# Kernel optimization log

Measured on AMD Instinct MI355X. Metric: run time of the kernel, lower is better.

## Reference

```python
import jax, jax.numpy as jnp
import numpy as np

N_HEAD = 8

def _l2norm(x, eps=1e-12):
    # F.normalize(p=2, dim=-1): x / max(||x||_2, eps)
    return x / jnp.maximum(jnp.linalg.norm(x, axis=-1, keepdims=True), eps)

def setup_inputs() -> dict:
    key = jax.random.key(0)
    ks = jax.random.split(key, 9)
    B, L, E = 2, 2048, 512
    s = 0.02
    return {
        "query": jax.random.normal(ks[0], (B, L, E), dtype=jnp.float32),
        "Wq": s * jax.random.normal(ks[1], (E, E), dtype=jnp.float32),
        "bq": jnp.zeros((E,), dtype=jnp.float32),
        "Wk": s * jax.random.normal(ks[2], (E, E), dtype=jnp.float32),
        "bk": jnp.zeros((E,), dtype=jnp.float32),
        "Wv": s * jax.random.normal(ks[3], (E, E), dtype=jnp.float32),
        "bv": jnp.zeros((E,), dtype=jnp.float32),
        "Wo": s * jax.random.normal(ks[4], (E, E), dtype=jnp.float32),
        "bo": jnp.zeros((E,), dtype=jnp.float32),
    }

def reference(query, Wq, bq, Wk, bk, Wv, bv, Wo, bo):
    B, L, E = query.shape
    H = N_HEAD
    hd = E // H
    # Faithful to torch: .view(tgt_len, bsz, E) is a RESHAPE, not a transpose.
    x = query.reshape(L, B, E)
    q = jax.nn.relu(x @ Wq.T + bq)
    k = jax.nn.relu(x @ Wk.T + bk)
    v = x @ Wv.T + bv
    q = _l2norm(q)
    k = _l2norm(k)
    # (L, B, E) -> (L, B*H, hd) -> (B*H, L, hd)
    q_ = q.reshape(L, B * H, hd).transpose(1, 0, 2)
    k_ = k.reshape(L, B * H, hd).transpose(1, 0, 2)
    v_ = v.reshape(L, B * H, hd).transpose(1, 0, 2)
    # Causal linear attention: cumulative outer-product of k,v then contract with q.
    kv = jnp.einsum('nld,nlm->nldm', k_, v_)      # [B*H, L, hd, hd]
    kv_cum = jnp.cumsum(kv, axis=1)
    out = jnp.einsum('nld,nldm->nlm', q_, kv_cum)  # [B*H, L, hd]
    out = out.transpose(1, 0, 2).reshape(L, B, E)
    out = out @ Wo.T + bo
    return out.reshape(B, L, E)
```

## Files before the change

kernel.cpp:

```cpp
#include <hip/hip_runtime.h>
#include <hip/hip_bf16.h>

typedef __attribute__((ext_vector_type(8))) short short8;
typedef __attribute__((ext_vector_type(4))) float f32x4;
using bf16 = __hip_bfloat16;

__device__ __forceinline__ unsigned short f2bf(float f) {
    unsigned u = __float_as_uint(f);
    u += 0x7fff + ((u >> 16) & 1);
    return (unsigned short)(u >> 16);
}
__device__ __forceinline__ float bf2f(unsigned short s) {
    return __uint_as_float(((unsigned)s) << 16);
}
__device__ __forceinline__ void gl_lds16(const unsigned short* g, unsigned short* l) {
    __builtin_amdgcn_global_load_lds(
        (const __attribute__((address_space(1))) unsigned int*)g,
        (__attribute__((address_space(3))) unsigned int*)l, 16, 0, 0);
}


__global__ __launch_bounds__(256) void pack_kernel(
    const float* __restrict__ X, const float* __restrict__ Wq, const float* __restrict__ Wk,
    const float* __restrict__ Wv, const float* __restrict__ Wo,
    bf16* __restrict__ Xp, bf16* __restrict__ Wqp, bf16* __restrict__ Wkp,
    bf16* __restrict__ Wvp, bf16* __restrict__ Wop, float* __restrict__ ssq)
{
    __shared__ __align__(16) unsigned short sm[4096];
    int id = blockIdx.x;
    int tid = threadIdx.x;
    if (id < 8) {
        int zi = id * 1024 + tid * 4;
        *(float4*)&ssq[zi] = make_float4(0.f, 0.f, 0.f, 0.f);
    }
    const float* src; unsigned short* dst; int g, sc;
    if (id < 512) { src = X; dst = (unsigned short*)Xp; g = id >> 3; sc = id & 7; }
    else {
        int t = id - 512; int wsel = t >> 6; int u = t & 63;
        g = u >> 3; sc = u & 7;
        src = (wsel == 0) ? Wq : ((wsel == 1) ? Wk : ((wsel == 2) ? Wv : Wo));
        dst = (unsigned short*)((wsel == 0) ? Wqp : ((wsel == 1) ? Wkp : ((wsel == 2) ? Wvp : Wop)));
    }
    int r = tid >> 2, kq = tid & 3;
    const float* sp = src + (size_t)(g * 64 + r) * 512 + sc * 64 + kq * 16;
    #pragma unroll
    for (int i = 0; i < 4; ++i) {
        float4 v = *(const float4*)(sp + i * 4);
        int kk = kq * 16 + i * 4;
        int sl = kk >> 3, el = kk & 7;
        ushort4 u4;
        u4.x = f2bf(v.x); u4.y = f2bf(v.y); u4.z = f2bf(v.z); u4.w = f2bf(v.w);
        *(ushort4*)&sm[(sl * 64 + r) * 8 + el] = u4;
    }
    __syncthreads();
    unsigned short* dp = dst + (size_t)g * 32768 + sc * 4096;
    *(uint4*)(dp + tid * 16)     = *(const uint4*)&sm[tid * 16];
    *(uint4*)(dp + tid * 16 + 8) = *(const uint4*)&sm[tid * 16 + 8];
}

__global__ __launch_bounds__(256) void qkv_gemm_kernel(
    const bf16* __restrict__ Xp,
    const bf16* __restrict__ W0p, const bf16* __restrict__ W1p, const bf16* __restrict__ W2p,
    const float* __restrict__ b0, const float* __restrict__ b1, const float* __restrict__ b2,
    bf16* __restrict__ O0, bf16* __restrict__ O1, bf16* __restrict__ O2,
    float* __restrict__ ssq)
{
    __shared__ __align__(16) unsigned short smem[8192];
    unsigned short* As = smem;
    unsigned short* Bs = smem + 2048;
    int z = blockIdx.z;
    const unsigned short* Wg = (const unsigned short*)((z == 0) ? W0p : ((z == 1) ? W1p : W2p));
    const float* bias = (z == 0) ? b0 : ((z == 1) ? b1 : b2);
    unsigned short* Out = (unsigned short*)((z == 0) ? O0 : ((z == 1) ? O1 : O2));
    const unsigned short* Ag = (const unsigned short*)Xp;

    int g  = blockIdx.x;
    int gB = blockIdx.y * 2;
    int m0 = g * 64;
    int n0 = blockIdx.y * 128;
    int tid = threadIdx.x;
    int lane = tid & 63;
    int w = tid >> 6;
    int wm = (w >> 1) * 32;
    int wn = (w & 1) * 64;
    int fr = lane & 15, qf = lane >> 4;

    f32x4 zero4 = {0.f, 0.f, 0.f, 0.f};
    f32x4 acc[2][4];
    #pragma unroll
    for (int t = 0; t < 2; ++t)
        #pragma unroll
        for (int u = 0; u < 4; ++u) acc[t][u] = zero4;

    for (int kw = 0; kw < 16; ++kw) {
        int s0 = kw * 4;
        __syncthreads();
        gl_lds16(Ag + ((size_t)(g * 64 + s0 + w) * 64 + lane) * 8, As + w * 512);
        gl_lds16(Wg + ((size_t)(gB * 64 + s0 + w) * 64 + lane) * 8, Bs + w * 1024);
        gl_lds16(Wg + ((size_t)((gB + 1) * 64 + s0 + w) * 64 + lane) * 8, Bs + w * 1024 + 512);
        __syncthreads();
        short8 af[2], bfr[4];
        #pragma unroll
        for (int t = 0; t < 2; ++t) af[t] = *(const short8*)&As[(qf * 64 + wm + t * 16 + fr) * 8];
        #pragma unroll
        for (int u = 0; u < 4; ++u) bfr[u] = *(const short8*)&Bs[(qf * 128 + wn + u * 16 + fr) * 8];
        #pragma unroll
        for (int t = 0; t < 2; ++t)
            #pragma unroll
            for (int u = 0; u < 4; ++u)
                acc[t][u] = __builtin_amdgcn_mfma_f32_16x16x32_bf16(af[t], bfr[u], acc[t][u], 0, 0, 0);
    }

    bool relu = (z < 2);
    int rb = qf * 4;
    #pragma unroll
    for (int t = 0; t < 2; ++t)
        #pragma unroll
        for (int u = 0; u < 4; ++u) {
            float bv = bias[n0 + wn + u * 16 + fr];
            #pragma unroll
            for (int r = 0; r < 4; ++r) {
                float v = acc[t][u][r] + bv;
                if (relu) v = fmaxf(v, 0.f);
                acc[t][u][r] = v;
            }
        }
    if (relu) {
        #pragma unroll
        for (int t = 0; t < 2; ++t)
            #pragma unroll
            for (int r = 0; r < 4; ++r) {
                float s = 0.f;
                #pragma unroll
                for (int u = 0; u < 4; ++u) s += acc[t][u][r] * acc[t][u][r];
                #pragma unroll
                for (int off = 1; off < 16; off <<= 1) s += __shfl_xor(s, off, 64);
                if (fr == 0) atomicAdd(&ssq[z * 4096 + m0 + wm + t * 16 + rb + r], s);
            }
    }
    __syncthreads();
    #pragma unroll
    for (int t = 0; t < 2; ++t)
        #pragma unroll
        for (int u = 0; u < 4; ++u)
            #pragma unroll
            for (int r = 0; r < 4; ++r)
                smem[(wm + t * 16 + rb + r) * 128 + wn + u * 16 + fr] = f2bf(acc[t][u][r]);
    __syncthreads();
    #pragma unroll
    for (int rep = 0; rep < 4; ++rep) {
        int idx8 = rep * 256 + tid;
        int row = idx8 >> 4, col8 = (idx8 & 15) * 8;
        *(uint4*)(Out + (size_t)(m0 + row) * 512 + n0 + col8) = *(const uint4*)&smem[row * 128 + col8];
    }
}

__global__ __launch_bounds__(256) void chunk_kv_kernel(
    const bf16* __restrict__ Kb, const bf16* __restrict__ Vb,
    const float* __restrict__ ssq, float* __restrict__ ScT, bf16* __restrict__ Vt_g)
{
    int n = blockIdx.x >> 4, c = blockIdx.x & 15;
    int b = n >> 3, h = n & 7;
    __shared__ float Ks[64 * 64];
    __shared__ float Vs[64 * 64];
    const unsigned short* Kg = (const unsigned short*)Kb;
    const unsigned short* Vg = (const unsigned short*)Vb;
    int tid = threadIdx.x;
    int td = tid >> 4, tm = tid & 15;
    int d0 = td * 4, m0 = tm * 4;
    int vm = tid & 63, vj0 = (tid >> 6) * 16;
    float acc[4][4] = {};
    for (int half = 0; half < 2; ++half) {
        __syncthreads();
        #pragma unroll
        for (int rep = 0; rep < 4; ++rep) {
            int idx = rep * 1024 + tid * 4;
            int j = idx >> 6, d = idx & 63;
            int grow = (c * 128 + half * 64 + j) * 2 + b;
            ushort4 ku = *(const ushort4*)&Kg[(size_t)grow * 512 + h * 64 + d];
            ushort4 vu = *(const ushort4*)&Vg[(size_t)grow * 512 + h * 64 + d];
            float rk = 1.f / fmaxf(sqrtf(ssq[4096 + grow]), 1e-12f);
            *(float4*)&Ks[j * 64 + d] = make_float4(bf2f(ku.x), bf2f(ku.y), bf2f(ku.z), bf2f(ku.w));
            *(float4*)&Vs[j * 64 + d] = make_float4(bf2f(vu.x) * rk, bf2f(vu.y) * rk,
                                                    bf2f(vu.z) * rk, bf2f(vu.w) * rk);
        }
        __syncthreads();
        for (int j = 0; j < 64; ++j) {
            float4 kv = *(const float4*)&Ks[j * 64 + d0];
            float4 vv = *(const float4*)&Vs[j * 64 + m0];
            acc[0][0] += kv.x*vv.x; acc[0][1] += kv.x*vv.y; acc[0][2] += kv.x*vv.z; acc[0][3] += kv.x*vv.w;
            acc[1][0] += kv.y*vv.x; acc[1][1] += kv.y*vv.y; acc[1][2] += kv.y*vv.z; acc[1][3] += kv.y*vv.w;
            acc[2][0] += kv.z*vv.x; acc[2][1] += kv.z*vv.y; acc[2][2] += kv.z*vv.z; acc[2][3] += kv.z*vv.w;
            acc[3][0] += kv.w*vv.x; acc[3][1] += kv.w*vv.y; acc[3][2] += kv.w*vv.z; acc[3][3] += kv.w*vv.w;
        }
        unsigned short tmp[16];
        #pragma unroll
        for (int i = 0; i < 16; ++i) tmp[i] = f2bf(Vs[(vj0 + i) * 64 + vm]);
        size_t vtoff = (size_t)n * 131072 + (size_t)vm * 2048 + c * 128 + half * 64 + vj0;
        *(uint4*)((unsigned short*)Vt_g + vtoff)     = *(uint4*)&tmp[0];
        *(uint4*)((unsigned short*)Vt_g + vtoff + 8) = *(uint4*)&tmp[8];
    }
    float* outp = ScT + (size_t)blockIdx.x * 4096;
    #pragma unroll
    for (int j2 = 0; j2 < 4; ++j2) {
        float4 o4 = make_float4(acc[0][j2], acc[1][j2], acc[2][j2], acc[3][j2]);
        *(float4*)&outp[(m0 + j2) * 64 + d0] = o4;
    }
}

__global__ __launch_bounds__(256) void prefix_kernel(const float* __restrict__ ScT, bf16* __restrict__ SpT)
{
    int n = blockIdx.x >> 4;
    int idx = ((blockIdx.x & 15) << 8) + threadIdx.x;
    size_t base = (size_t)n * 65536 + idx;
    unsigned short* sp = (unsigned short*)SpT;
    float run = 0.f;
    #pragma unroll
    for (int c = 0; c < 16; ++c) {
        size_t off = base + (size_t)c * 4096;
        sp[off] = f2bf(run);
        run += ScT[off];
    }
}

__global__ __launch_bounds__(256) void attn_kernel(
    const bf16* __restrict__ Qb, const bf16* __restrict__ Kb,
    const bf16* __restrict__ Vt_g, const bf16* __restrict__ SpT_g,
    const float* __restrict__ ssq, bf16* __restrict__ AOb)
{
    int n = blockIdx.x >> 4, c = blockIdx.x & 15;
    int b = n >> 3, h = n & 7;
    __shared__ unsigned short Qs[128 * 72];
    __shared__ unsigned short Ks[128 * 72];
    __shared__ unsigned short Vt[64 * 136];
    __shared__ unsigned short Ps[4 * 32 * 40];
    int tid = threadIdx.x;
    int lane = tid & 63;
    int w = tid >> 6;
    int fr = lane & 15, q = lane >> 4;

    const unsigned short* Qg = (const unsigned short*)Qb;
    const unsigned short* Kg = (const unsigned short*)Kb;
    const unsigned short* Vg = (const unsigned short*)Vt_g;

    #pragma unroll
    for (int rep = 0; rep < 4; ++rep) {
        int idx = rep * 256 + tid;
        int l = idx >> 3, dc = (idx & 7) * 8;
        size_t goff = (size_t)((c * 128 + l) * 2 + b) * 512 + h * 64 + dc;
        *(uint4*)&Qs[l * 72 + dc] = *(const uint4*)(Qg + goff);
        *(uint4*)&Ks[l * 72 + dc] = *(const uint4*)(Kg + goff);
    }
    #pragma unroll
    for (int rep = 0; rep < 4; ++rep) {
        int idx = rep * 256 + tid;
        int m = idx >> 4, jc = (idx & 15) * 8;
        *(uint4*)&Vt[m * 136 + jc] =
            *(const uint4*)(Vg + (size_t)n * 131072 + (size_t)m * 2048 + c * 128 + jc);
    }
    __syncthreads();

    short8 qf[2][2];
    #pragma unroll
    for (int lt = 0; lt < 2; ++lt)
        #pragma unroll
        for (int kh = 0; kh < 2; ++kh)
            qf[lt][kh] = *(const short8*)&Qs[(w * 32 + lt * 16 + fr) * 72 + kh * 32 + q * 8];

    f32x4 zero4 = {0.f, 0.f, 0.f, 0.f};
    f32x4 oacc[2][4];
    #pragma unroll
    for (int lt = 0; lt < 2; ++lt)
        #pragma unroll
        for (int mt = 0; mt < 4; ++mt) oacc[lt][mt] = zero4;

    const unsigned short* spg = (const unsigned short*)SpT_g + (size_t)blockIdx.x * 4096;
    #pragma unroll
    for (int mt = 0; mt < 4; ++mt) {
        #pragma unroll
        for (int kh = 0; kh < 2; ++kh) {
            short8 sf = *(const short8*)&spg[(mt * 16 + fr) * 64 + kh * 32 + q * 8];
            oacc[0][mt] = __builtin_amdgcn_mfma_f32_16x16x32_bf16(qf[0][kh], sf, oacc[0][mt], 0, 0, 0);
            oacc[1][mt] = __builtin_amdgcn_mfma_f32_16x16x32_bf16(qf[1][kh], sf, oacc[1][mt], 0, 0, 0);
        }
    }

    unsigned short* myPs = &Ps[w * 1280];
    int rbase = q * 4;
    for (int jt = 0; jt <= w; ++jt) {
        f32x4 pacc[2][2];
        pacc[0][0] = zero4; pacc[0][1] = zero4; pacc[1][0] = zero4; pacc[1][1] = zero4;
        #pragma unroll
        for (int jt16 = 0; jt16 < 2; ++jt16) {
            #pragma unroll
            for (int kh = 0; kh < 2; ++kh) {
                short8 kf = *(const short8*)&Ks[(jt * 32 + jt16 * 16 + fr) * 72 + kh * 32 + q * 8];
                pacc[0][jt16] = __builtin_amdgcn_mfma_f32_16x16x32_bf16(qf[0][kh], kf, pacc[0][jt16], 0, 0, 0);
                pacc[1][jt16] = __builtin_amdgcn_mfma_f32_16x16x32_bf16(qf[1][kh], kf, pacc[1][jt16], 0, 0, 0);
            }
        }
        bool diag = (jt == w);
        #pragma unroll
        for (int lt = 0; lt < 2; ++lt)
            #pragma unroll
            for (int jt16 = 0; jt16 < 2; ++jt16)
                #pragma unroll
                for (int r = 0; r < 4; ++r) {
                    int ll = lt * 16 + rbase + r;
                    int jl = jt16 * 16 + fr;
                    float pv = pacc[lt][jt16][r];
                    if (diag && jl > ll) pv = 0.f;
                    myPs[ll * 40 + jl] = f2bf(pv);
                }
        short8 pf0 = *(const short8*)&myPs[fr * 40 + q * 8];
        short8 pf1 = *(const short8*)&myPs[(16 + fr) * 40 + q * 8];
        #pragma unroll
        for (int mt = 0; mt < 4; ++mt) {
            short8 vf = *(const short8*)&Vt[(mt * 16 + fr) * 136 + jt * 32 + q * 8];
            oacc[0][mt] = __builtin_amdgcn_mfma_f32_16x16x32_bf16(pf0, vf, oacc[0][mt], 0, 0, 0);
            oacc[1][mt] = __builtin_amdgcn_mfma_f32_16x16x32_bf16(pf1, vf, oacc[1][mt], 0, 0, 0);
        }
    }

    float rqv[2][4];
    #pragma unroll
    for (int lt = 0; lt < 2; ++lt)
        #pragma unroll
        for (int r = 0; r < 4; ++r) {
            int flat = (c * 128 + w * 32 + lt * 16 + rbase + r) * 2 + b;
            rqv[lt][r] = 1.f / fmaxf(sqrtf(ssq[flat]), 1e-12f);
        }
    __syncthreads();
    #pragma unroll
    for (int lt = 0; lt < 2; ++lt)
        #pragma unroll
        for (int mt = 0; mt < 4; ++mt)
            #pragma unroll
            for (int r = 0; r < 4; ++r)
                Qs[(w * 32 + lt * 16 + rbase + r) * 64 + mt * 16 + fr] = f2bf(oacc[lt][mt][r] * rqv[lt][r]);
    __syncthreads();
    #pragma unroll
    for (int rep = 0; rep < 4; ++rep) {
        int idx8 = rep * 256 + tid;
        int l = idx8 >> 3, m8 = (idx8 & 7) * 8;
        *(uint4*)((unsigned short*)AOb + (size_t)((c * 128 + l) * 2 + b) * 512 + h * 64 + m8) =
            *(const uint4*)&Qs[l * 64 + m8];
    }
}

__global__ __launch_bounds__(256) void oproj_kernel(
    const bf16* __restrict__ A, const bf16* __restrict__ Wop,
    const float* __restrict__ bias, float* __restrict__ Out)
{
    __shared__ __align__(16) unsigned short smem[16384];
    unsigned short* As = smem;
    unsigned short* Bs = smem + 2560;
    const unsigned short* Ag = (const unsigned short*)A;
    const unsigned short* Wg = (const unsigned short*)Wop;
    int m0 = blockIdx.x * 64;
    int gB = blockIdx.y * 2;
    int n0 = blockIdx.y * 128;
    int tid = threadIdx.x;
    int lane = tid & 63;
    int w = tid >> 6;
    int fr = lane & 15, qf = lane >> 4;
    int wm = (w >> 1) * 32;
    int wn = (w & 1) * 64;
    int srow = tid >> 2;
    int skk  = (tid & 3) * 8;

    f32x4 zero4 = {0.f, 0.f, 0.f, 0.f};
    f32x4 acc[2][4];
    #pragma unroll
    for (int t = 0; t < 2; ++t)
        #pragma unroll
        for (int u = 0; u < 4; ++u) acc[t][u] = zero4;

    for (int kw = 0; kw < 16; ++kw) {
        int k0 = kw * 32, s0 = kw * 4;
        __syncthreads();
        *(uint4*)&As[srow * 40 + skk] = *(const uint4*)(Ag + (size_t)(m0 + srow) * 512 + k0 + skk);
        gl_lds16(Wg + ((size_t)(gB * 64 + s0 + w) * 64 + lane) * 8, Bs + w * 1024);
        gl_lds16(Wg + ((size_t)((gB + 1) * 64 + s0 + w) * 64 + lane) * 8, Bs + w * 1024 + 512);
        __syncthreads();
        short8 af[2], bfr[4];
        #pragma unroll
        for (int t = 0; t < 2; ++t) af[t] = *(const short8*)&As[(wm + t * 16 + fr) * 40 + qf * 8];
        #pragma unroll
        for (int u = 0; u < 4; ++u) bfr[u] = *(const short8*)&Bs[(qf * 128 + wn + u * 16 + fr) * 8];
        #pragma unroll
        for (int t = 0; t < 2; ++t)
            #pragma unroll
            for (int u = 0; u < 4; ++u)
                acc[t][u] = __builtin_amdgcn_mfma_f32_16x16x32_bf16(af[t], bfr[u], acc[t][u], 0, 0, 0);
    }

    int rb = qf * 4;
    float* Cf = (float*)smem;
    __syncthreads();
    #pragma unroll
    for (int t = 0; t < 2; ++t)
        #pragma unroll
        for (int u = 0; u < 4; ++u) {
            float bv = bias[n0 + wn + u * 16 + fr];
            #pragma unroll
            for (int r = 0; r < 4; ++r)
                Cf[(wm + t * 16 + rb + r) * 128 + wn + u * 16 + fr] = acc[t][u][r] + bv;
        }
    __syncthreads();
    #pragma unroll
    for (int rep = 0; rep < 8; ++rep) {
        int idx = rep * 256 + tid;
        int row = idx >> 5, c4 = (idx & 31) * 4;
        *(float4*)(Out + (size_t)(m0 + row) * 512 + n0 + c4) = *(const float4*)&Cf[row * 128 + c4];
    }
}

extern "C" void kernel_launch(void* const* d_in, const int* in_sizes, int n_in,
                              void* d_out, int out_size, void* d_ws, size_t ws_size,
                              hipStream_t stream)
{
    (void)in_sizes; (void)n_in; (void)out_size; (void)ws_size;
    const float* x  = (const float*)d_in[0];
    const float* Wq = (const float*)d_in[1];
    const float* bq = (const float*)d_in[2];
    const float* Wk = (const float*)d_in[3];
    const float* bk = (const float*)d_in[4];
    const float* Wv = (const float*)d_in[5];
    const float* bv = (const float*)d_in[6];
    const float* Wo = (const float*)d_in[7];
    const float* bo = (const float*)d_in[8];
    float* out = (float*)d_out;

    float* ssq = (float*)d_ws;
    bf16* Xp  = (bf16*)(ssq + 8192);
    bf16* Wqp = Xp + 2097152;
    bf16* Wkp = Wqp + 262144;
    bf16* Wvp = Wkp + 262144;
    bf16* Wop = Wvp + 262144;
    bf16* Qb  = Wop + 262144;
    bf16* Kb  = Qb + 2097152;
    bf16* Vb  = Kb + 2097152;
    bf16* Vt  = Vb + 2097152;
    bf16* AOb = Vt + 2097152;
    bf16* SpT = AOb + 2097152;
    float* ScT = (float*)(SpT + 1048576);

    pack_kernel<<<768, 256, 0, stream>>>(x, Wq, Wk, Wv, Wo, Xp, Wqp, Wkp, Wvp, Wop, ssq);
    qkv_gemm_kernel<<<dim3(64, 4, 3), 256, 0, stream>>>(Xp, Wqp, Wkp, Wvp, bq, bk, bv, Qb, Kb, Vb, ssq);
    chunk_kv_kernel<<<dim3(256), 256, 0, stream>>>(Kb, Vb, ssq, ScT, Vt);
    prefix_kernel<<<dim3(256), 256, 0, stream>>>(ScT, SpT);
    attn_kernel<<<dim3(256), 256, 0, stream>>>(Qb, Kb, Vt, SpT, ssq, AOb);
    oproj_kernel<<<dim3(64, 4), 256, 0, stream>>>(AOb, Wop, bo, out);
}
```

Baseline: 123.6 us.

## Fuse QKV projections per block and fold prefix scan into attention kernel

The QKV GEMM now computes all three projections in one block, sharing each loaded X tile across Wq, Wk and Wv. That cuts A-tile reloads and the grid from 768 to 256 blocks, at the cost of three times the accumulator registers. The separate prefix-sum kernel is removed; each attention block instead sums the preceding chunk states directly from fp32 ScT. This saves a launch and an intermediate bf16 buffer but adds redundant loads that grow with the chunk index.

```diff
diff --git a/kernel.cpp b/kernel.cpp
--- a/kernel.cpp
+++ b/kernel.cpp
@@ -65,14 +65,11 @@
     bf16* __restrict__ O0, bf16* __restrict__ O1, bf16* __restrict__ O2,
     float* __restrict__ ssq)
 {
-    __shared__ __align__(16) unsigned short smem[8192];
-    unsigned short* As = smem;
-    unsigned short* Bs = smem + 2048;
-    int z = blockIdx.z;
-    const unsigned short* Wg = (const unsigned short*)((z == 0) ? W0p : ((z == 1) ? W1p : W2p));
-    const float* bias = (z == 0) ? b0 : ((z == 1) ? b1 : b2);
-    unsigned short* Out = (unsigned short*)((z == 0) ? O0 : ((z == 1) ? O1 : O2));
+    __shared__ __align__(16) unsigned short SM[14336];
+    unsigned short* As = SM;
     const unsigned short* Ag = (const unsigned short*)Xp;
+    const unsigned short* Wg[3] = { (const unsigned short*)W0p, (const unsigned short*)W1p,
+                                    (const unsigned short*)W2p };
 
     int g  = blockIdx.x;
     int gB = blockIdx.y * 2;
@@ -83,75 +80,90 @@
     int w = tid >> 6;
     int wm = (w >> 1) * 32;
     int wn = (w & 1) * 64;
-    int fr = lane & 15, qf = lane >> 4;
+    int fr = lane & 15, q = lane >> 4;
 
     f32x4 zero4 = {0.f, 0.f, 0.f, 0.f};
-    f32x4 acc[2][4];
-    #pragma unroll
-    for (int t = 0; t < 2; ++t)
-        #pragma unroll
-        for (int u = 0; u < 4; ++u) acc[t][u] = zero4;
+    f32x4 acc[3][2][4];
+    #pragma unroll
+    for (int z = 0; z < 3; ++z)
+        #pragma unroll
+        for (int t = 0; t < 2; ++t)
+            #pragma unroll
+            for (int u = 0; u < 4; ++u) acc[z][t][u] = zero4;
 
     for (int kw = 0; kw < 16; ++kw) {
         int s0 = kw * 4;
         __syncthreads();
         gl_lds16(Ag + ((size_t)(g * 64 + s0 + w) * 64 + lane) * 8, As + w * 512);
-        gl_lds16(Wg + ((size_t)(gB * 64 + s0 + w) * 64 + lane) * 8, Bs + w * 1024);
-        gl_lds16(Wg + ((size_t)((gB + 1) * 64 + s0 + w) * 64 + lane) * 8, Bs + w * 1024 + 512);
-        __syncthreads();
-        short8 af[2], bfr[4];
-        #pragma unroll
-        for (int t = 0; t < 2; ++t) af[t] = *(const short8*)&As[(qf * 64 + wm + t * 16 + fr) * 8];
-        #pragma unroll
-        for (int u = 0; u < 4; ++u) bfr[u] = *(const short8*)&Bs[(qf * 128 + wn + u * 16 + fr) * 8];
+        #pragma unroll
+        for (int z = 0; z < 3; ++z) {
+            unsigned short* Bz = SM + 2048 + z * 4096;
+            gl_lds16(Wg[z] + ((size_t)(gB * 64 + s0 + w) * 64 + lane) * 8, Bz + w * 1024);
+            gl_lds16(Wg[z] + ((size_t)((gB + 1) * 64 + s0 + w) * 64 + lane) * 8, Bz + w * 1024 + 512);
+        }
+        __syncthreads();
+        short8 af[2];
+        #pragma unroll
+        for (int t = 0; t < 2; ++t) af[t] = *(const short8*)&As[(q * 64 + wm + t * 16 + fr) * 8];
+        #pragma unroll
+        for (int z = 0; z < 3; ++z) {
+            unsigned short* Bz = SM + 2048 + z * 4096;
+            short8 bfr[4];
+            #pragma unroll
+            for (int u = 0; u < 4; ++u) bfr[u] = *(const short8*)&Bz[(q * 128 + wn + u * 16 + fr) * 8];
+            #pragma unroll
+            for (int t = 0; t < 2; ++t)
+                #pragma unroll
+                for (int u = 0; u < 4; ++u)
+                    acc[z][t][u] = __builtin_amdgcn_mfma_f32_16x16x32_bf16(af[t], bfr[u], acc[z][t][u], 0, 0, 0);
+        }
+    }
+
+    int rb = q * 4;
+    for (int z = 0; z < 3; ++z) {
+        const float* bias = (z == 0) ? b0 : ((z == 1) ? b1 : b2);
+        unsigned short* Out = (unsigned short*)((z == 0) ? O0 : ((z == 1) ? O1 : O2));
+        bool relu = (z < 2);
         #pragma unroll
         for (int t = 0; t < 2; ++t)
             #pragma unroll
+            for (int u = 0; u < 4; ++u) {
+                float bv = bias[n0 + wn + u * 16 + fr];
+                #pragma unroll
+                for (int r = 0; r < 4; ++r) {
+                    float v = acc[z][t][u][r] + bv;
+                    if (relu) v = fmaxf(v, 0.f);
+                    acc[z][t][u][r] = v;
+                }
+            }
+        if (relu) {
+            #pragma unroll
+            for (int t = 0; t < 2; ++t)
+                #pragma unroll
+                for (int r = 0; r < 4; ++r) {
+                    float s = 0.f;
+                    #pragma unroll
+                    for (int u = 0; u < 4; ++u) s += acc[z][t][u][r] * acc[z][t][u][r];
+                    #pragma unroll
+                    for (int off = 1; off < 16; off <<= 1) s += __shfl_xor(s, off, 64);
+                    if (fr == 0) atomicAdd(&ssq[z * 4096 + m0 + wm + t * 16 + rb + r], s);
+                }
+        }
+        __syncthreads();
+        #pragma unroll
+        for (int t = 0; t < 2; ++t)
+            #pragma unroll
             for (int u = 0; u < 4; ++u)
-                acc[t][u] = __builtin_amdgcn_mfma_f32_16x16x32_bf16(af[t], bfr[u], acc[t][u], 0, 0, 0);
-    }
-
-    bool relu = (z < 2);
-    int rb = qf * 4;
-    #pragma unroll
-    for (int t = 0; t < 2; ++t)
-        #pragma unroll
-        for (int u = 0; u < 4; ++u) {
-            float bv = bias[n0 + wn + u * 16 + fr];
-            #pragma unroll
-            for (int r = 0; r < 4; ++r) {
-                float v = acc[t][u][r] + bv;
-                if (relu) v = fmaxf(v, 0.f);
-                acc[t][u][r] = v;
-            }
-        }
-    if (relu) {
-        #pragma unroll
-        for (int t = 0; t < 2; ++t)
-            #pragma unroll
-            for (int r = 0; r < 4; ++r) {
-                float s = 0.f;
                 #pragma unroll
-                for (int u = 0; u < 4; ++u) s += acc[t][u][r] * acc[t][u][r];
-                #pragma unroll
-                for (int off = 1; off < 16; off <<= 1) s += __shfl_xor(s, off, 64);
-                if (fr == 0) atomicAdd(&ssq[z * 4096 + m0 + wm + t * 16 + rb + r], s);
-            }
-    }
-    __syncthreads();
-    #pragma unroll
-    for (int t = 0; t < 2; ++t)
-        #pragma unroll
-        for (int u = 0; u < 4; ++u)
-            #pragma unroll
-            for (int r = 0; r < 4; ++r)
-                smem[(wm + t * 16 + rb + r) * 128 + wn + u * 16 + fr] = f2bf(acc[t][u][r]);
-    __syncthreads();
-    #pragma unroll
-    for (int rep = 0; rep < 4; ++rep) {
-        int idx8 = rep * 256 + tid;
-        int row = idx8 >> 4, col8 = (idx8 & 15) * 8;
-        *(uint4*)(Out + (size_t)(m0 + row) * 512 + n0 + col8) = *(const uint4*)&smem[row * 128 + col8];
+                for (int r = 0; r < 4; ++r)
+                    SM[(wm + t * 16 + rb + r) * 128 + wn + u * 16 + fr] = f2bf(acc[z][t][u][r]);
+        __syncthreads();
+        #pragma unroll
+        for (int rep = 0; rep < 4; ++rep) {
+            int idx8 = rep * 256 + tid;
+            int row = idx8 >> 4, col8 = (idx8 & 15) * 8;
+            *(uint4*)(Out + (size_t)(m0 + row) * 512 + n0 + col8) = *(const uint4*)&SM[row * 128 + col8];
+        }
     }
 }
 
@@ -208,24 +220,9 @@
     }
 }
 
-__global__ __launch_bounds__(256) void prefix_kernel(const float* __restrict__ ScT, bf16* __restrict__ SpT)
-{
-    int n = blockIdx.x >> 4;
-    int idx = ((blockIdx.x & 15) << 8) + threadIdx.x;
-    size_t base = (size_t)n * 65536 + idx;
-    unsigned short* sp = (unsigned short*)SpT;
-    float run = 0.f;
-    #pragma unroll
-    for (int c = 0; c < 16; ++c) {
-        size_t off = base + (size_t)c * 4096;
-        sp[off] = f2bf(run);
-        run += ScT[off];
-    }
-}
-
 __global__ __launch_bounds__(256) void attn_kernel(
     const bf16* __restrict__ Qb, const bf16* __restrict__ Kb,
-    const bf16* __restrict__ Vt_g, const bf16* __restrict__ SpT_g,
+    const bf16* __restrict__ Vt_g, const float* __restrict__ ScT,
     const float* __restrict__ ssq, bf16* __restrict__ AOb)
 {
     int n = blockIdx.x >> 4, c = blockIdx.x & 15;
@@ -274,12 +271,23 @@
         #pragma unroll
         for (int mt = 0; mt < 4; ++mt) oacc[lt][mt] = zero4;
 
-    const unsigned short* spg = (const unsigned short*)SpT_g + (size_t)blockIdx.x * 4096;
+    const float* scb = ScT + (size_t)(n * 16) * 4096;
     #pragma unroll
     for (int mt = 0; mt < 4; ++mt) {
         #pragma unroll
         for (int kh = 0; kh < 2; ++kh) {
-            short8 sf = *(const short8*)&spg[(mt * 16 + fr) * 64 + kh * 32 + q * 8];
+            float sp[8] = {0.f,0.f,0.f,0.f,0.f,0.f,0.f,0.f};
+            int eo = (mt * 16 + fr) * 64 + kh * 32 + q * 8;
+            for (int cp = 0; cp < c; ++cp) {
+                float4 a = *(const float4*)&scb[cp * 4096 + eo];
+                float4 d = *(const float4*)&scb[cp * 4096 + eo + 4];
+                sp[0]+=a.x; sp[1]+=a.y; sp[2]+=a.z; sp[3]+=a.w;
+                sp[4]+=d.x; sp[5]+=d.y; sp[6]+=d.z; sp[7]+=d.w;
+            }
+            unsigned short su[8];
+            #pragma unroll
+            for (int e = 0; e < 8; ++e) su[e] = f2bf(sp[e]);
+            short8 sf = *(const short8*)su;
             oacc[0][mt] = __builtin_amdgcn_mfma_f32_16x16x32_bf16(qf[0][kh], sf, oacc[0][mt], 0, 0, 0);
             oacc[1][mt] = __builtin_amdgcn_mfma_f32_16x16x32_bf16(qf[1][kh], sf, oacc[1][mt], 0, 0, 0);
         }
@@ -443,13 +451,11 @@
     bf16* Vb  = Kb + 2097152;
     bf16* Vt  = Vb + 2097152;
     bf16* AOb = Vt + 2097152;
-    bf16* SpT = AOb + 2097152;
-    float* ScT = (float*)(SpT + 1048576);
+    float* ScT = (float*)(AOb + 2097152);
 
     pack_kernel<<<768, 256, 0, stream>>>(x, Wq, Wk, Wv, Wo, Xp, Wqp, Wkp, Wvp, Wop, ssq);
-    qkv_gemm_kernel<<<dim3(64, 4, 3), 256, 0, stream>>>(Xp, Wqp, Wkp, Wvp, bq, bk, bv, Qb, Kb, Vb, ssq);
+    qkv_gemm_kernel<<<dim3(64, 4), 256, 0, stream>>>(Xp, Wqp, Wkp, Wvp, bq, bk, bv, Qb, Kb, Vb, ssq);
     chunk_kv_kernel<<<dim3(256), 256, 0, stream>>>(Kb, Vb, ssq, ScT, Vt);
-    prefix_kernel<<<dim3(256), 256, 0, stream>>>(ScT, SpT);
-    attn_kernel<<<dim3(256), 256, 0, stream>>>(Qb, Kb, Vt, SpT, ssq, AOb);
+    attn_kernel<<<dim3(256), 256, 0, stream>>>(Qb, Kb, Vt, ScT, ssq, AOb);
     oproj_kernel<<<dim3(64, 4), 256, 0, stream>>>(AOb, Wop, bo, out);
 }
```

New measurement: 157.3 us. +27.2%, slower.

## Halve attention chunk size to 64 and shrink oproj tiles to double grid size

Applied to the files above, without the earlier changes.

Changes the causal linear-attention chunk length from 128 to 64 rows, so the chunk-KV and attention kernels launch 512 blocks instead of 256 and the prefix scan runs over 32 chunk states. The attention kernel now has each wave handle 16 query rows with a smaller intra-chunk causal block. The output projection tile shrinks from 64x128 to 64x64, doubling its grid. The aim is better occupancy across the many CUs of the GPU, at the cost of twice as much chunk-state traffic and a longer serial prefix loop.

```diff
diff --git a/kernel.cpp b/kernel.cpp
--- a/kernel.cpp
+++ b/kernel.cpp
@@ -159,7 +159,7 @@
     const bf16* __restrict__ Kb, const bf16* __restrict__ Vb,
     const float* __restrict__ ssq, float* __restrict__ ScT, bf16* __restrict__ Vt_g)
 {
-    int n = blockIdx.x >> 4, c = blockIdx.x & 15;
+    int n = blockIdx.x >> 5, c = blockIdx.x & 31;
     int b = n >> 3, h = n & 7;
     __shared__ float Ks[64 * 64];
     __shared__ float Vs[64 * 64];
@@ -168,38 +168,36 @@
     int tid = threadIdx.x;
     int td = tid >> 4, tm = tid & 15;
     int d0 = td * 4, m0 = tm * 4;
+    #pragma unroll
+    for (int rep = 0; rep < 4; ++rep) {
+        int idx = rep * 1024 + tid * 4;
+        int j = idx >> 6, d = idx & 63;
+        int grow = (c * 64 + j) * 2 + b;
+        ushort4 ku = *(const ushort4*)&Kg[(size_t)grow * 512 + h * 64 + d];
+        ushort4 vu = *(const ushort4*)&Vg[(size_t)grow * 512 + h * 64 + d];
+        float rk = 1.f / fmaxf(sqrtf(ssq[4096 + grow]), 1e-12f);
+        *(float4*)&Ks[j * 64 + d] = make_float4(bf2f(ku.x), bf2f(ku.y), bf2f(ku.z), bf2f(ku.w));
+        *(float4*)&Vs[j * 64 + d] = make_float4(bf2f(vu.x) * rk, bf2f(vu.y) * rk,
+                                                bf2f(vu.z) * rk, bf2f(vu.w) * rk);
+    }
+    __syncthreads();
+    float acc[4][4] = {};
+    for (int j = 0; j < 64; ++j) {
+        float4 kv = *(const float4*)&Ks[j * 64 + d0];
+        float4 vv = *(const float4*)&Vs[j * 64 + m0];
+        acc[0][0] += kv.x*vv.x; acc[0][1] += kv.x*vv.y; acc[0][2] += kv.x*vv.z; acc[0][3] += kv.x*vv.w;
+        acc[1][0] += kv.y*vv.x; acc[1][1] += kv.y*vv.y; acc[1][2] += kv.y*vv.z; acc[1][3] += kv.y*vv.w;
+        acc[2][0] += kv.z*vv.x; acc[2][1] += kv.z*vv.y; acc[2][2] += kv.z*vv.z; acc[2][3] += kv.z*vv.w;
+        acc[3][0] += kv.w*vv.x; acc[3][1] += kv.w*vv.y; acc[3][2] += kv.w*vv.z; acc[3][3] += kv.w*vv.w;
+    }
     int vm = tid & 63, vj0 = (tid >> 6) * 16;
-    float acc[4][4] = {};
-    for (int half = 0; half < 2; ++half) {
-        __syncthreads();
-        #pragma unroll
-        for (int rep = 0; rep < 4; ++rep) {
-            int idx = rep * 1024 + tid * 4;
-            int j = idx >> 6, d = idx & 63;
-            int grow = (c * 128 + half * 64 + j) * 2 + b;
-            ushort4 ku = *(const ushort4*)&Kg[(size_t)grow * 512 + h * 64 + d];
-            ushort4 vu = *(const ushort4*)&Vg[(size_t)grow * 512 + h * 64 + d];
-            float rk = 1.f / fmaxf(sqrtf(ssq[4096 + grow]), 1e-12f);
-            *(float4*)&Ks[j * 64 + d] = make_float4(bf2f(ku.x), bf2f(ku.y), bf2f(ku.z), bf2f(ku.w));
-            *(float4*)&Vs[j * 64 + d] = make_float4(bf2f(vu.x) * rk, bf2f(vu.y) * rk,
-                                                    bf2f(vu.z) * rk, bf2f(vu.w) * rk);
-        }
-        __syncthreads();
-        for (int j = 0; j < 64; ++j) {
-            float4 kv = *(const float4*)&Ks[j * 64 + d0];
-            float4 vv = *(const float4*)&Vs[j * 64 + m0];
-            acc[0][0] += kv.x*vv.x; acc[0][1] += kv.x*vv.y; acc[0][2] += kv.x*vv.z; acc[0][3] += kv.x*vv.w;
-            acc[1][0] += kv.y*vv.x; acc[1][1] += kv.y*vv.y; acc[1][2] += kv.y*vv.z; acc[1][3] += kv.y*vv.w;
-            acc[2][0] += kv.z*vv.x; acc[2][1] += kv.z*vv.y; acc[2][2] += kv.z*vv.z; acc[2][3] += kv.z*vv.w;
-            acc[3][0] += kv.w*vv.x; acc[3][1] += kv.w*vv.y; acc[3][2] += kv.w*vv.z; acc[3][3] += kv.w*vv.w;
-        }
-        unsigned short tmp[16];
-        #pragma unroll
-        for (int i = 0; i < 16; ++i) tmp[i] = f2bf(Vs[(vj0 + i) * 64 + vm]);
-        size_t vtoff = (size_t)n * 131072 + (size_t)vm * 2048 + c * 128 + half * 64 + vj0;
-        *(uint4*)((unsigned short*)Vt_g + vtoff)     = *(uint4*)&tmp[0];
-        *(uint4*)((unsigned short*)Vt_g + vtoff + 8) = *(uint4*)&tmp[8];
-    }
+    unsigned short tmp[16];
+    #pragma unroll
+    for (int i = 0; i < 16; ++i) tmp[i] = f2bf(Vs[(vj0 + i) * 64 + vm]);
+    size_t vtoff = (size_t)n * 131072 + (size_t)vm * 2048 + c * 64 + vj0;
+    *(uint4*)((unsigned short*)Vt_g + vtoff)     = *(uint4*)&tmp[0];
+    *(uint4*)((unsigned short*)Vt_g + vtoff + 8) = *(uint4*)&tmp[8];
+
     float* outp = ScT + (size_t)blockIdx.x * 4096;
     #pragma unroll
     for (int j2 = 0; j2 < 4; ++j2) {
@@ -212,11 +210,11 @@
 {
     int n = blockIdx.x >> 4;
     int idx = ((blockIdx.x & 15) << 8) + threadIdx.x;
-    size_t base = (size_t)n * 65536 + idx;
+    size_t base = (size_t)n * 131072 + idx;
     unsigned short* sp = (unsigned short*)SpT;
     float run = 0.f;
     #pragma unroll
-    for (int c = 0; c < 16; ++c) {
+    for (int c = 0; c < 32; ++c) {
         size_t off = base + (size_t)c * 4096;
         sp[off] = f2bf(run);
         run += ScT[off];
@@ -228,12 +226,12 @@
     const bf16* __restrict__ Vt_g, const bf16* __restrict__ SpT_g,
     const float* __restrict__ ssq, bf16* __restrict__ AOb)
 {
-    int n = blockIdx.x >> 4, c = blockIdx.x & 15;
+    int n = blockIdx.x >> 5, c = blockIdx.x & 31;
     int b = n >> 3, h = n & 7;
-    __shared__ unsigned short Qs[128 * 72];
-    __shared__ unsigned short Ks[128 * 72];
-    __shared__ unsigned short Vt[64 * 136];
-    __shared__ unsigned short Ps[4 * 32 * 40];
+    __shared__ unsigned short Qs[64 * 72];
+    __shared__ unsigned short Ks[64 * 72];
+    __shared__ unsigned short Vt[64 * 72];
+    __shared__ unsigned short Ps[4 * 16 * 40];
     int tid = threadIdx.x;
     int lane = tid & 63;
     int w = tid >> 6;
@@ -244,35 +242,27 @@
     const unsigned short* Vg = (const unsigned short*)Vt_g;
 
     #pragma unroll
-    for (int rep = 0; rep < 4; ++rep) {
+    for (int rep = 0; rep < 2; ++rep) {
         int idx = rep * 256 + tid;
         int l = idx >> 3, dc = (idx & 7) * 8;
-        size_t goff = (size_t)((c * 128 + l) * 2 + b) * 512 + h * 64 + dc;
+        size_t goff = (size_t)((c * 64 + l) * 2 + b) * 512 + h * 64 + dc;
         *(uint4*)&Qs[l * 72 + dc] = *(const uint4*)(Qg + goff);
         *(uint4*)&Ks[l * 72 + dc] = *(const uint4*)(Kg + goff);
-    }
-    #pragma unroll
-    for (int rep = 0; rep < 4; ++rep) {
-        int idx = rep * 256 + tid;
-        int m = idx >> 4, jc = (idx & 15) * 8;
-        *(uint4*)&Vt[m * 136 + jc] =
-            *(const uint4*)(Vg + (size_t)n * 131072 + (size_t)m * 2048 + c * 128 + jc);
-    }
-    __syncthreads();
-
-    short8 qf[2][2];
-    #pragma unroll
-    for (int lt = 0; lt < 2; ++lt)
-        #pragma unroll
-        for (int kh = 0; kh < 2; ++kh)
-            qf[lt][kh] = *(const short8*)&Qs[(w * 32 + lt * 16 + fr) * 72 + kh * 32 + q * 8];
+        int m = l, jc = dc;
+        *(uint4*)&Vt[m * 72 + jc] =
+            *(const uint4*)(Vg + (size_t)n * 131072 + (size_t)m * 2048 + c * 64 + jc);
+    }
+    __syncthreads();
+
+    short8 qf[2];
+    #pragma unroll
+    for (int kh = 0; kh < 2; ++kh)
+        qf[kh] = *(const short8*)&Qs[(w * 16 + fr) * 72 + kh * 32 + q * 8];
 
     f32x4 zero4 = {0.f, 0.f, 0.f, 0.f};
-    f32x4 oacc[2][4];
-    #pragma unroll
-    for (int lt = 0; lt < 2; ++lt)
-        #pragma unroll
-        for (int mt = 0; mt < 4; ++mt) oacc[lt][mt] = zero4;
+    f32x4 oacc[4];
+    #pragma unroll
+    for (int mt = 0; mt < 4; ++mt) oacc[mt] = zero4;
 
     const unsigned short* spg = (const unsigned short*)SpT_g + (size_t)blockIdx.x * 4096;
     #pragma unroll
@@ -280,70 +270,61 @@
         #pragma unroll
         for (int kh = 0; kh < 2; ++kh) {
             short8 sf = *(const short8*)&spg[(mt * 16 + fr) * 64 + kh * 32 + q * 8];
-            oacc[0][mt] = __builtin_amdgcn_mfma_f32_16x16x32_bf16(qf[0][kh], sf, oacc[0][mt], 0, 0, 0);
-            oacc[1][mt] = __builtin_amdgcn_mfma_f32_16x16x32_bf16(qf[1][kh], sf, oacc[1][mt], 0, 0, 0);
+            oacc[mt] = __builtin_amdgcn_mfma_f32_16x16x32_bf16(qf[kh], sf, oacc[mt], 0, 0, 0);
         }
     }
 
-    unsigned short* myPs = &Ps[w * 1280];
+    unsigned short* myPs = &Ps[w * 640];
     int rbase = q * 4;
-    for (int jt = 0; jt <= w; ++jt) {
-        f32x4 pacc[2][2];
-        pacc[0][0] = zero4; pacc[0][1] = zero4; pacc[1][0] = zero4; pacc[1][1] = zero4;
+    int njt = (w >> 1) + 1;
+    for (int jt = 0; jt < njt; ++jt) {
+        f32x4 pacc[2];
+        pacc[0] = zero4; pacc[1] = zero4;
         #pragma unroll
         for (int jt16 = 0; jt16 < 2; ++jt16) {
             #pragma unroll
             for (int kh = 0; kh < 2; ++kh) {
                 short8 kf = *(const short8*)&Ks[(jt * 32 + jt16 * 16 + fr) * 72 + kh * 32 + q * 8];
-                pacc[0][jt16] = __builtin_amdgcn_mfma_f32_16x16x32_bf16(qf[0][kh], kf, pacc[0][jt16], 0, 0, 0);
-                pacc[1][jt16] = __builtin_amdgcn_mfma_f32_16x16x32_bf16(qf[1][kh], kf, pacc[1][jt16], 0, 0, 0);
+                pacc[jt16] = __builtin_amdgcn_mfma_f32_16x16x32_bf16(qf[kh], kf, pacc[jt16], 0, 0, 0);
             }
         }
-        bool diag = (jt == w);
-        #pragma unroll
-        for (int lt = 0; lt < 2; ++lt)
-            #pragma unroll
-            for (int jt16 = 0; jt16 < 2; ++jt16)
-                #pragma unroll
-                for (int r = 0; r < 4; ++r) {
-                    int ll = lt * 16 + rbase + r;
-                    int jl = jt16 * 16 + fr;
-                    float pv = pacc[lt][jt16][r];
-                    if (diag && jl > ll) pv = 0.f;
-                    myPs[ll * 40 + jl] = f2bf(pv);
-                }
-        short8 pf0 = *(const short8*)&myPs[fr * 40 + q * 8];
-        short8 pf1 = *(const short8*)&myPs[(16 + fr) * 40 + q * 8];
+        bool diag = (jt == njt - 1);
+        int lloc = w * 16 + rbase;
+        #pragma unroll
+        for (int jt16 = 0; jt16 < 2; ++jt16)
+            #pragma unroll
+            for (int r = 0; r < 4; ++r) {
+                int jl = jt * 32 + jt16 * 16 + fr;
+                float pv = pacc[jt16][r];
+                if (diag && jl > lloc + r) pv = 0.f;
+                myPs[(rbase + r) * 40 + jt16 * 16 + fr] = f2bf(pv);
+            }
+        short8 pf = *(const short8*)&myPs[fr * 40 + q * 8];
         #pragma unroll
         for (int mt = 0; mt < 4; ++mt) {
-            short8 vf = *(const short8*)&Vt[(mt * 16 + fr) * 136 + jt * 32 + q * 8];
-            oacc[0][mt] = __builtin_amdgcn_mfma_f32_16x16x32_bf16(pf0, vf, oacc[0][mt], 0, 0, 0);
-            oacc[1][mt] = __builtin_amdgcn_mfma_f32_16x16x32_bf16(pf1, vf, oacc[1][mt], 0, 0, 0);
+            short8 vf = *(const short8*)&Vt[(mt * 16 + fr) * 72 + jt * 32 + q * 8];
+            oacc[mt] = __builtin_amdgcn_mfma_f32_16x16x32_bf16(pf, vf, oacc[mt], 0, 0, 0);
         }
     }
 
-    float rqv[2][4];
-    #pragma unroll
-    for (int lt = 0; lt < 2; ++lt)
-        #pragma unroll
-        for (int r = 0; r < 4; ++r) {
-            int flat = (c * 128 + w * 32 + lt * 16 + rbase + r) * 2 + b;
-            rqv[lt][r] = 1.f / fmaxf(sqrtf(ssq[flat]), 1e-12f);
-        }
-    __syncthreads();
-    #pragma unroll
-    for (int lt = 0; lt < 2; ++lt)
-        #pragma unroll
-        for (int mt = 0; mt < 4; ++mt)
-            #pragma unroll
-            for (int r = 0; r < 4; ++r)
-                Qs[(w * 32 + lt * 16 + rbase + r) * 64 + mt * 16 + fr] = f2bf(oacc[lt][mt][r] * rqv[lt][r]);
-    __syncthreads();
-    #pragma unroll
-    for (int rep = 0; rep < 4; ++rep) {
+    float rqv[4];
+    #pragma unroll
+    for (int r = 0; r < 4; ++r) {
+        int flat = (c * 64 + w * 16 + rbase + r) * 2 + b;
+        rqv[r] = 1.f / fmaxf(sqrtf(ssq[flat]), 1e-12f);
+    }
+    __syncthreads();
+    #pragma unroll
+    for (int mt = 0; mt < 4; ++mt)
+        #pragma unroll
+        for (int r = 0; r < 4; ++r)
+            Qs[(w * 16 + rbase + r) * 64 + mt * 16 + fr] = f2bf(oacc[mt][r] * rqv[r]);
+    __syncthreads();
+    #pragma unroll
+    for (int rep = 0; rep < 2; ++rep) {
         int idx8 = rep * 256 + tid;
         int l = idx8 >> 3, m8 = (idx8 & 7) * 8;
-        *(uint4*)((unsigned short*)AOb + (size_t)((c * 128 + l) * 2 + b) * 512 + h * 64 + m8) =
+        *(uint4*)((unsigned short*)AOb + (size_t)((c * 64 + l) * 2 + b) * 512 + h * 64 + m8) =
             *(const uint4*)&Qs[l * 64 + m8];
     }
 }
@@ -352,47 +333,43 @@
     const bf16* __restrict__ A, const bf16* __restrict__ Wop,
     const float* __restrict__ bias, float* __restrict__ Out)
 {
-    __shared__ __align__(16) unsigned short smem[16384];
+    __shared__ __align__(16) unsigned short smem[8192];
     unsigned short* As = smem;
     unsigned short* Bs = smem + 2560;
     const unsigned short* Ag = (const unsigned short*)A;
     const unsigned short* Wg = (const unsigned short*)Wop;
     int m0 = blockIdx.x * 64;
-    int gB = blockIdx.y * 2;
-    int n0 = blockIdx.y * 128;
+    int gy = blockIdx.y;
+    int n0 = gy * 64;
     int tid = threadIdx.x;
     int lane = tid & 63;
     int w = tid >> 6;
     int fr = lane & 15, qf = lane >> 4;
     int wm = (w >> 1) * 32;
-    int wn = (w & 1) * 64;
+    int wn = (w & 1) * 32;
     int srow = tid >> 2;
     int skk  = (tid & 3) * 8;
 
     f32x4 zero4 = {0.f, 0.f, 0.f, 0.f};
-    f32x4 acc[2][4];
-    #pragma unroll
-    for (int t = 0; t < 2; ++t)
-        #pragma unroll
-        for (int u = 0; u < 4; ++u) acc[t][u] = zero4;
+    f32x4 acc[2][2];
+    acc[0][0] = zero4; acc[0][1] = zero4; acc[1][0] = zero4; acc[1][1] = zero4;
 
     for (int kw = 0; kw < 16; ++kw) {
         int k0 = kw * 32, s0 = kw * 4;
         __syncthreads();
         *(uint4*)&As[srow * 40 + skk] = *(const uint4*)(Ag + (size_t)(m0 + srow) * 512 + k0 + skk);
-        gl_lds16(Wg + ((size_t)(gB * 64 + s0 + w) * 64 + lane) * 8, Bs + w * 1024);
-        gl_lds16(Wg + ((size_t)((gB + 1) * 64 + s0 + w) * 64 + lane) * 8, Bs + w * 1024 + 512);
+        gl_lds16(Wg + ((size_t)(gy * 64 + s0 + w) * 64 + lane) * 8, Bs + w * 512);
         __syncthreads();
-        short8 af[2], bfr[4];
+        short8 af[2], bf[2];
         #pragma unroll
         for (int t = 0; t < 2; ++t) af[t] = *(const short8*)&As[(wm + t * 16 + fr) * 40 + qf * 8];
         #pragma unroll
-        for (int u = 0; u < 4; ++u) bfr[u] = *(const short8*)&Bs[(qf * 128 + wn + u * 16 + fr) * 8];
+        for (int u = 0; u < 2; ++u) bf[u] = *(const short8*)&Bs[(qf * 64 + wn + u * 16 + fr) * 8];
         #pragma unroll
         for (int t = 0; t < 2; ++t)
             #pragma unroll
-            for (int u = 0; u < 4; ++u)
-                acc[t][u] = __builtin_amdgcn_mfma_f32_16x16x32_bf16(af[t], bfr[u], acc[t][u], 0, 0, 0);
+            for (int u = 0; u < 2; ++u)
+                acc[t][u] = __builtin_amdgcn_mfma_f32_16x16x32_bf16(af[t], bf[u], acc[t][u], 0, 0, 0);
     }
 
     int rb = qf * 4;
@@ -401,18 +378,18 @@
     #pragma unroll
     for (int t = 0; t < 2; ++t)
         #pragma unroll
-        for (int u = 0; u < 4; ++u) {
+        for (int u = 0; u < 2; ++u) {
             float bv = bias[n0 + wn + u * 16 + fr];
             #pragma unroll
             for (int r = 0; r < 4; ++r)
-                Cf[(wm + t * 16 + rb + r) * 128 + wn + u * 16 + fr] = acc[t][u][r] + bv;
+                Cf[(wm + t * 16 + rb + r) * 64 + wn + u * 16 + fr] = acc[t][u][r] + bv;
         }
     __syncthreads();
     #pragma unroll
-    for (int rep = 0; rep < 8; ++rep) {
+    for (int rep = 0; rep < 4; ++rep) {
         int idx = rep * 256 + tid;
-        int row = idx >> 5, c4 = (idx & 31) * 4;
-        *(float4*)(Out + (size_t)(m0 + row) * 512 + n0 + c4) = *(const float4*)&Cf[row * 128 + c4];
+        int row = idx >> 4, c4 = (idx & 15) * 4;
+        *(float4*)(Out + (size_t)(m0 + row) * 512 + n0 + c4) = *(const float4*)&Cf[row * 64 + c4];
     }
 }
 
@@ -444,12 +421,12 @@
     bf16* Vt  = Vb + 2097152;
     bf16* AOb = Vt + 2097152;
     bf16* SpT = AOb + 2097152;
-    float* ScT = (float*)(SpT + 1048576);
+    float* ScT = (float*)(SpT + 2097152);
 
     pack_kernel<<<768, 256, 0, stream>>>(x, Wq, Wk, Wv, Wo, Xp, Wqp, Wkp, Wvp, Wop, ssq);
     qkv_gemm_kernel<<<dim3(64, 4, 3), 256, 0, stream>>>(Xp, Wqp, Wkp, Wvp, bq, bk, bv, Qb, Kb, Vb, ssq);
-    chunk_kv_kernel<<<dim3(256), 256, 0, stream>>>(Kb, Vb, ssq, ScT, Vt);
+    chunk_kv_kernel<<<dim3(512), 256, 0, stream>>>(Kb, Vb, ssq, ScT, Vt);
     prefix_kernel<<<dim3(256), 256, 0, stream>>>(ScT, SpT);
-    attn_kernel<<<dim3(256), 256, 0, stream>>>(Qb, Kb, Vt, SpT, ssq, AOb);
-    oproj_kernel<<<dim3(64, 4), 256, 0, stream>>>(AOb, Wop, bo, out);
-}
+    attn_kernel<<<dim3(512), 256, 0, stream>>>(Qb, Kb, Vt, SpT, ssq, AOb);
+    oproj_kernel<<<dim3(64, 8), 256, 0, stream>>>(AOb, Wop, bo, out);
+}
```

Measured after the change: 122.7 us (median of 2 runs). About the same (-0.8%).
